# Kernel optimization log

Measured on AMD Instinct MI355X. Metric: run time of the kernel, lower is better.

Reference implementation:

```python
import jax, jax.numpy as jnp
import numpy as np

N = 50000      # total nodes in batched graph
E = 800000     # total edges (avg degree 16)
B = 512        # number of graphs in batch
F_IN = 74      # input node feature size
H = 64         # hidden size per layer
OUT = 64       # output_feats
EPS = 1e-5     # BatchNorm eps


def setup_inputs() -> dict:
    key = jax.random.key(0)
    ks = jax.random.split(key, 32)
    d = {}
    d['feats'] = jax.random.normal(ks[0], (N, F_IN), dtype=jnp.float32)
    d['src'] = jax.random.randint(ks[1], (E,), 0, N)
    d['dst'] = jax.random.randint(ks[2], (E,), 0, N)
    d['graph_ids'] = jnp.sort(jax.random.randint(ks[3], (N,), 0, B))
    dims = [F_IN, H, H, H]
    i = 4
    for l in range(3):
        din, dout = dims[l], dims[l + 1]
        d[f'W{l}'] = jax.random.normal(ks[i], (din, dout), jnp.float32) / np.sqrt(din).astype(np.float32); i += 1
        d[f'b{l}'] = jnp.zeros((dout,), jnp.float32)
        d[f'rW{l}'] = jax.random.normal(ks[i], (din, dout), jnp.float32) / np.sqrt(din).astype(np.float32); i += 1
        d[f'rb{l}'] = jnp.zeros((dout,), jnp.float32)
        d[f'g{l}'] = jnp.ones((dout,), jnp.float32)    # BN gamma
        d[f'be{l}'] = jnp.zeros((dout,), jnp.float32)  # BN beta
    d['aw_W'] = jax.random.normal(ks[i], (H, 1), jnp.float32) / np.sqrt(H).astype(np.float32); i += 1
    d['aw_b'] = jnp.zeros((1,), jnp.float32)
    d['out_W'] = jax.random.normal(ks[i], (2 * H, OUT), jnp.float32) / np.sqrt(2 * H).astype(np.float32); i += 1
    d['out_b'] = jnp.zeros((OUT,), jnp.float32)
    return d


def _gcn_layer(x, src, dst, W, b, rW, rb, g, be):
    # GraphConv, norm='none': out = sum-aggregate(X W) + b, then relu
    xw = x @ W                                                    # [N, dout]
    agg = jax.ops.segment_sum(xw[src], dst, num_segments=N) + b   # gather/scatter over edges
    h = jax.nn.relu(agg)
    # residual: relu(Linear(x))
    h = h + jax.nn.relu(x @ rW + rb)
    # dropout p=0 -> identity
    # BatchNorm1d (training-mode batch statistics, biased variance)
    mean = jnp.mean(h, axis=0)
    var = jnp.var(h, axis=0)
    return (h - mean) * jax.lax.rsqrt(var + EPS) * g + be


def reference(feats, src, dst, graph_ids,
              W0, b0, rW0, rb0, g0, be0,
              W1, b1, rW1, rb1, g1, be1,
              W2, b2, rW2, rb2, g2, be2,
              aw_W, aw_b, out_W, out_b):
    h = feats
    h = _gcn_layer(h, src, dst, W0, b0, rW0, rb0, g0, be0)
    h = _gcn_layer(h, src, dst, W1, b1, rW1, rb1, g1, be1)
    h = _gcn_layer(h, src, dst, W2, b2, rW2, rb2, g2, be2)
    # WeightedSumAndMax readout
    w = jax.nn.sigmoid(h @ aw_W + aw_b)                               # [N, 1]
    h_sum = jax.ops.segment_sum(h * w, graph_ids, num_segments=B)     # [B, H]
    h_max = jax.ops.segment_max(h, graph_ids, num_segments=B)         # [B, H]
    h_max = jnp.where(jnp.isfinite(h_max), h_max, 0.0)                # empty graphs -> 0 (dgl max_nodes)
    h_g = jnp.concatenate([h_sum, h_max], axis=1)                     # [B, 2H]
    return h_g @ out_W + out_b                                        # [B, OUT]
```

## Files before the change

kernel.cpp:

```cpp
#include <hip/hip_runtime.h>
#include <hip/hip_bf16.h>
#include <math.h>

#define NN 50000
#define NE 800000
#define NB 512
#define FIN 74
#define HD 64
#define BN_EPS 1e-5f

#define SCHUNK 512
#define NCHUNK ((NN + SCHUNK - 1) / SCHUNK)

#define CHUNK 32
#define ELLW 32
#define NBLK ((NN + CHUNK - 1) / CHUNK)


__global__ void csr_zero_kernel(int* __restrict__ cnt, int* __restrict__ cnt2,
                                float* __restrict__ stats012,
                                unsigned long long* __restrict__ xw_zrow,
                                const float* __restrict__ W0, const float* __restrict__ rW0,
                                float2* __restrict__ Wpk0) {
    int i = blockIdx.x * 256 + threadIdx.x;
    if (i < NN) { cnt[i] = 0; cnt2[i] = 0; }
    if (i < 384) stats012[i] = 0.f;
    if (i < 16) xw_zrow[i] = 0ull;
    if (i < FIN * HD) Wpk0[i] = make_float2(W0[i], rW0[i]);
}

__global__ void csr_hist_kernel(const int* __restrict__ dst, int* __restrict__ cnt) {
    int e = blockIdx.x * 256 + threadIdx.x;
    if (e < NE) atomicAdd(&cnt[dst[e]], 1);
}

__global__ void scanA_kernel(const int* __restrict__ cnt, int* __restrict__ bsum) {
    __shared__ int l[SCHUNK];
    int i = blockIdx.x * SCHUNK + threadIdx.x;
    int v = (i < NN) ? cnt[i] : 0;
    l[threadIdx.x] = v;
    __syncthreads();
    for (int off = SCHUNK / 2; off; off >>= 1) {
        if (threadIdx.x < off) l[threadIdx.x] += l[threadIdx.x + off];
        __syncthreads();
    }
    if (threadIdx.x == 0) bsum[blockIdx.x] = l[0];
}

__global__ void scanB_kernel(int* __restrict__ bsum) {
    int lane = threadIdx.x;
    int v0 = (lane < NCHUNK) ? bsum[lane] : 0;
    int v1 = (64 + lane < NCHUNK) ? bsum[64 + lane] : 0;
    int s0 = v0, s1 = v1;
    for (int off = 1; off < 64; off <<= 1) {
        int t0 = __shfl_up(s0, off, 64);
        int t1 = __shfl_up(s1, off, 64);
        if (lane >= off) { s0 += t0; s1 += t1; }
    }
    int tot0 = __shfl(s0, 63, 64);
    if (lane < NCHUNK) bsum[lane] = s0 - v0;
    if (64 + lane < NCHUNK) bsum[64 + lane] = s1 - v1 + tot0;
}

__global__ void scanC_kernel(const int* __restrict__ cnt, const int* __restrict__ bsum,
                             int* __restrict__ row_ptr) {
    __shared__ int l[SCHUNK];
    int i = blockIdx.x * SCHUNK + threadIdx.x;
    int v = (i < NN) ? cnt[i] : 0;
    l[threadIdx.x] = v;
    __syncthreads();
    for (int off = 1; off < SCHUNK; off <<= 1) {
        int t = (threadIdx.x >= off) ? l[threadIdx.x - off] : 0;
        __syncthreads();
        l[threadIdx.x] += t;
        __syncthreads();
    }
    int excl = l[threadIdx.x] - v + bsum[blockIdx.x];
    if (i < NN) row_ptr[i] = excl;
    if (i == NN - 1) row_ptr[NN] = excl + v;
}

__global__ void csr_fill_kernel(const int* __restrict__ src, const int* __restrict__ dst,
                                const int* __restrict__ row_ptr, int* __restrict__ cnt2,
                                int* __restrict__ eidx) {
    int i = blockIdx.x * 256 + threadIdx.x;
    if (i < NE) {
        int d = dst[i];
        int p = row_ptr[d] + atomicAdd(&cnt2[d], 1);
        eidx[p] = src[i];
    }
}


template <int K>
__global__ __launch_bounds__(256) void gemm_dual_kernel(
    const float* __restrict__ x, const float2* __restrict__ Wpk,
    const float* __restrict__ rb, __hip_bfloat16* __restrict__ xw,
    __hip_bfloat16* __restrict__ res, int n) {
    __shared__ float2 sW[K * HD];
    __shared__ float srb[64];
    for (int i = threadIdx.x; i < K * HD; i += 256) sW[i] = Wpk[i];
    if (threadIdx.x < 64) srb[threadIdx.x] = rb[threadIdx.x];
    __syncthreads();
    int wl = threadIdx.x >> 6, lane = threadIdx.x & 63;
    for (int r0 = (blockIdx.x * 4 + wl) * 8; r0 < n; r0 += gridDim.x * 32) {
        float a1[8], a2[8];
#pragma unroll
        for (int r = 0; r < 8; ++r) { a1[r] = 0.f; a2[r] = 0.f; }
#pragma unroll
        for (int c0 = 0; c0 < K; c0 += 64) {
            const int cl = (K - c0 < 64) ? (K - c0) : 64;
            float xv[8];
#pragma unroll
            for (int r = 0; r < 8; ++r) {
                int row = r0 + r;
                xv[r] = (lane < cl && row < n) ? x[(size_t)row * K + c0 + lane] : 0.f;
            }
            for (int j = 0; j < cl; ++j) {
                float2 w = sW[(c0 + j) * HD + lane];
#pragma unroll
                for (int r = 0; r < 8; ++r) {
                    float xb = __uint_as_float(
                        __builtin_amdgcn_readlane(__float_as_uint(xv[r]), j));
                    a1[r] = fmaf(xb, w.x, a1[r]);
                    a2[r] = fmaf(xb, w.y, a2[r]);
                }
            }
        }
#pragma unroll
        for (int r = 0; r < 8; ++r) {
            int row = r0 + r;
            if (row < n) {
                xw[(size_t)row * HD + lane] = __float2bfloat16(a1[r]);
                res[(size_t)row * HD + lane] = __float2bfloat16(fmaxf(a2[r] + srb[lane], 0.f));
            }
        }
    }
}

__global__ void fold_kernel(const float* __restrict__ stats, const float* __restrict__ g,
                            const float* __restrict__ be, const float* __restrict__ W,
                            const float* __restrict__ rW, const float* __restrict__ rb,
                            float2* __restrict__ Wpk, float* __restrict__ shiftW,
                            float* __restrict__ rbp) {
    __shared__ float sc[64], sh[64];
    int t = threadIdx.x;
    if (t < 64) {
        float mean = stats[t] / (float)NN;
        float var = stats[64 + t] / (float)NN - mean * mean;
        float scale = g[t] * rsqrtf(var + BN_EPS);
        sc[t] = scale;
        sh[t] = be[t] - mean * scale;
    }
    __syncthreads();
    for (int i = t; i < 64 * 64; i += 256) {
        int k = i >> 6;
        Wpk[i] = make_float2(sc[k] * W[i], sc[k] * rW[i]);
    }
    if (t < 64) {
        float sw = 0.f, srw = 0.f;
        for (int k = 0; k < 64; ++k) {
            sw = fmaf(sh[k], W[k * 64 + t], sw);
            srw = fmaf(sh[k], rW[k * 64 + t], srw);
        }
        shiftW[t] = sw;
        rbp[t] = rb[t] + srw;
    }
}

__device__ __forceinline__ float bf_lo(unsigned int p) { return __uint_as_float(p << 16); }
__device__ __forceinline__ float bf_hi(unsigned int p) { return __uint_as_float(p & 0xffff0000u); }

__global__ __launch_bounds__(256) void fused_agg_kernel(
    const __hip_bfloat16* __restrict__ xw, const __hip_bfloat16* __restrict__ res,
    const float* __restrict__ b, const float* __restrict__ shiftW,
    const int* __restrict__ row_ptr, const int* __restrict__ geidx,
    float* __restrict__ hout, float* __restrict__ stats, int n) {
    __shared__ int sIdx[CHUNK][ELLW];
    __shared__ int sRP[CHUNK + 1];
    __shared__ int sLen[CHUNK];
    __shared__ float sbb[128];
    __shared__ float lsr[256 * 4];

    int tid = threadIdx.x;
    int r0 = blockIdx.x * CHUNK;

    if (tid <= CHUNK) {
        int rp = r0 + tid;
        sRP[tid] = row_ptr[(rp < NN) ? rp : NN];
    }
    if (tid >= 128 && tid < 256) {
        int j = tid - 128;
        sbb[j] = (j < 64) ? b[j] : (shiftW ? shiftW[j - 64] : 0.f);
    }
    __syncthreads();
    for (int i = tid; i < CHUNK * ELLW; i += 256) {
        int r = i >> 5, j = i & 31;
        int beg = sRP[r];
        int plen = sRP[r + 1] - beg;
        sIdx[r][j] = (j < plen) ? geidx[beg + j] : NN;
        if (j == 0) sLen[r] = plen;
    }
    __syncthreads();

    const unsigned* XWdw = (const unsigned*)xw;
    const unsigned* REdw = (const unsigned*)res;
    int wl = tid >> 6, lane = tid & 63;
    int c2 = lane & 31, half = lane >> 5;
    float sb0 = sbb[2 * c2], sb1 = sbb[2 * c2 + 1];
    float sw0 = sbb[64 + 2 * c2], sw1 = sbb[64 + 2 * c2 + 1];
    float s0 = 0.f, s1 = 0.f, q0 = 0.f, q1 = 0.f;

#pragma unroll
    for (int p = 0; p < 4; ++p) {
        int rA = wl * 8 + 2 * p;
        int rloc = rA + half;
        int grow = r0 + rloc;
        int growc = (grow < n) ? grow : (n - 1);
        int lenA = sLen[rA], lenB = sLen[rA + 1];
        int kmax = (lenA > lenB) ? lenA : lenB;
        int mylen = half ? lenB : lenA;
        unsigned rdw = REdw[(size_t)growc * 32 + c2];
        float a0 = 0.f, a1 = 0.f;
        int klim = (kmax < ELLW) ? kmax : ELLW;
        for (int k8 = 0; k8 < klim; k8 += 8) {
#pragma unroll
            for (int j = 0; j < 8; ++j) {
                int idx = sIdx[rloc][k8 + j];
                unsigned dw = XWdw[(size_t)idx * 32 + c2];
                a0 += bf_lo(dw);
                a1 += bf_hi(dw);
            }
        }
        if (kmax > ELLW) {
            int beg = sRP[rloc];
            for (int k = ELLW; k < kmax; ++k) {
                int idx = geidx[beg + k];
                unsigned dw = XWdw[(size_t)((k < mylen) ? idx : NN) * 32 + c2];
                a0 += bf_lo(dw);
                a1 += bf_hi(dw);
            }
        }
        float dg = (float)mylen;
        float hv0 = fmaxf(a0 + fmaf(dg, sw0, sb0), 0.f) + bf_lo(rdw);
        float hv1 = fmaxf(a1 + fmaf(dg, sw1, sb1), 0.f) + bf_hi(rdw);
        if (grow < n) {
            *(float2*)&hout[(size_t)grow * HD + 2 * c2] = make_float2(hv0, hv1);
            s0 += hv0; s1 += hv1;
            q0 += hv0 * hv0; q1 += hv1 * hv1;
        }
    }

    lsr[tid * 4 + 0] = s0;
    lsr[tid * 4 + 1] = s1;
    lsr[tid * 4 + 2] = q0;
    lsr[tid * 4 + 3] = q1;
    __syncthreads();
    if (tid < 64) {
        int comp = tid & 1, c2i = tid >> 1;
        float ss = 0.f, qq = 0.f;
#pragma unroll
        for (int w = 0; w < 4; ++w)
#pragma unroll
            for (int h = 0; h < 2; ++h) {
                int t = w * 64 + h * 32 + c2i;
                ss += lsr[t * 4 + comp];
                qq += lsr[t * 4 + 2 + comp];
            }
        atomicAdd(&stats[tid], ss);
        atomicAdd(&stats[64 + tid], qq);
    }
}


__global__ void readout_init_kernel(float* __restrict__ hsum, unsigned int* __restrict__ hmax,
                                    const float* __restrict__ stats, const float* __restrict__ g,
                                    const float* __restrict__ be, float* __restrict__ ss) {
    int idx = blockIdx.x * 256 + threadIdx.x;
    if (idx < NB * HD) {
        hsum[idx] = 0.f;
        hmax[idx] = 0x007FFFFFu;
    }
    if (blockIdx.x == 0 && threadIdx.x < 64) {
        int c = threadIdx.x;
        float mean = stats[c] / (float)NN;
        float var = stats[64 + c] / (float)NN - mean * mean;
        float scale = g[c] * rsqrtf(var + BN_EPS);
        ss[c] = scale;
        ss[64 + c] = be[c] - mean * scale;
    }
}

#define RNODES 16

__device__ __forceinline__ void ro_flush(float* hsum, unsigned int* hmax, int g, int c,
                                         float accS, float accM) {
    atomicAdd(&hsum[g * HD + c], accS);
    unsigned int bits = __float_as_uint(accM);
    unsigned int enc = (bits & 0x80000000u) ? ~bits : (bits | 0x80000000u);
    atomicMax(&hmax[g * HD + c], enc);
}

__global__ __launch_bounds__(256) void readout_kernel(
    const float* __restrict__ h, const int* __restrict__ gid, const float* __restrict__ ss,
    const float* __restrict__ awW, const float* __restrict__ awb, float* __restrict__ hsum,
    unsigned int* __restrict__ hmax, int n) {
    int wid = blockIdx.x * 4 + (threadIdx.x >> 6);
    int c = threadIdx.x & 63;
    int r0 = wid * RNODES;
    if (r0 >= n) return;
    int r1 = r0 + RNODES;
    if (r1 > n) r1 = n;
    float aw = awW[c], ab = awb[0];
    float sA = ss[c], sB = ss[64 + c];
    int cur = gid[r0];
    float accS = 0.f, accM = -__builtin_inff();
    for (int r = r0; r < r1; ++r) {
        int g = gid[r];
        if (g != cur) {
            ro_flush(hsum, hmax, cur, c, accS, accM);
            accS = 0.f;
            accM = -__builtin_inff();
            cur = g;
        }
        float v = fmaf(h[(size_t)r * HD + c], sA, sB);
        float p = v * aw;
        for (int off = 32; off; off >>= 1) p += __shfl_xor(p, off, 64);
        float w = 1.f / (1.f + expf(-(p + ab)));
        accS = fmaf(v, w, accS);
        accM = fmaxf(accM, v);
    }
    ro_flush(hsum, hmax, cur, c, accS, accM);
}

__global__ void final_kernel(const float* __restrict__ hsum, const unsigned int* __restrict__ hmax,
                             const float* __restrict__ outW, const float* __restrict__ outb,
                             float* __restrict__ out) {
    __shared__ float sW[128 * 64];
    for (int i = threadIdx.x; i < 128 * 64; i += 256) sW[i] = outW[i];
    __syncthreads();
    int idx = blockIdx.x * 256 + threadIdx.x;
    if (idx >= NB * HD) return;
    int bi = idx >> 6, o = idx & 63;
    float acc = outb[o];
#pragma unroll 4
    for (int k = 0; k < 64; ++k) acc = fmaf(hsum[bi * 64 + k], sW[k * 64 + o], acc);
#pragma unroll 4
    for (int k = 0; k < 64; ++k) {
        unsigned int e = hmax[bi * 64 + k];
        float m;
        if (e == 0x007FFFFFu) {
            m = 0.f;
        } else {
            m = (e & 0x80000000u) ? __uint_as_float(e ^ 0x80000000u) : __uint_as_float(~e);
        }
        acc = fmaf(m, sW[(64 + k) * 64 + o], acc);
    }
    out[idx] = acc;
}


extern "C" void kernel_launch(void* const* d_in, const int* in_sizes, int n_in,
                              void* d_out, int out_size, void* d_ws, size_t ws_size,
                              hipStream_t stream) {
    const float* feats = (const float*)d_in[0];
    const int* src = (const int*)d_in[1];
    const int* dst = (const int*)d_in[2];
    const int* gid = (const int*)d_in[3];
    const float* W[3];
    const float* b[3];
    const float* rW[3];
    const float* rb[3];
    const float* g[3];
    const float* be[3];
    for (int l = 0; l < 3; ++l) {
        W[l] = (const float*)d_in[4 + 6 * l + 0];
        b[l] = (const float*)d_in[4 + 6 * l + 1];
        rW[l] = (const float*)d_in[4 + 6 * l + 2];
        rb[l] = (const float*)d_in[4 + 6 * l + 3];
        g[l] = (const float*)d_in[4 + 6 * l + 4];
        be[l] = (const float*)d_in[4 + 6 * l + 5];
    }
    const float* awW = (const float*)d_in[22];
    const float* awb = (const float*)d_in[23];
    const float* outW = (const float*)d_in[24];
    const float* outb = (const float*)d_in[25];
    float* out = (float*)d_out;

    __hip_bfloat16* XW = (__hip_bfloat16*)d_ws;
    __hip_bfloat16* RES = XW + (size_t)(NN + 1) * HD;
    float* P1 = (float*)(RES + (size_t)NN * HD);
    float* stats = P1 + (size_t)NN * HD;
    float* ss2 = stats + 384;
    float2* WPK = (float2*)(ss2 + 128);
    float* shW = (float*)(WPK + FIN * HD);
    float* rbp = shW + 64;
    float* hsum = rbp + 64;
    unsigned int* hmax = (unsigned int*)(hsum + (size_t)NB * HD);
    int* cnt = (int*)(hmax + (size_t)NB * HD);
    int* cnt2 = cnt + NN;
    int* row_ptr = cnt2 + NN;
    int* bsum = row_ptr + NN + 1;
    int* eidx = bsum + NCHUNK;

    float* stats0 = stats;
    float* stats1 = stats + 128;
    float* stats2 = stats + 256;

    const int EBLK = (NE + 255) / 256;
    const int GEMMBLK = 640;
    const int ROBLK = (NN + RNODES * 4 - 1) / (RNODES * 4);

    csr_zero_kernel<<<(NN + 255) / 256, 256, 0, stream>>>(
        cnt, cnt2, stats, (unsigned long long*)(XW + (size_t)NN * HD), W[0], rW[0], WPK);
    csr_hist_kernel<<<EBLK, 256, 0, stream>>>(dst, cnt);
    scanA_kernel<<<NCHUNK, SCHUNK, 0, stream>>>(cnt, bsum);
    scanB_kernel<<<1, 64, 0, stream>>>(bsum);
    scanC_kernel<<<NCHUNK, SCHUNK, 0, stream>>>(cnt, bsum, row_ptr);
    csr_fill_kernel<<<EBLK, 256, 0, stream>>>(src, dst, row_ptr, cnt2, eidx);

    gemm_dual_kernel<FIN><<<GEMMBLK, 256, 0, stream>>>(feats, WPK, rb[0], XW, RES, NN);
    fused_agg_kernel<<<NBLK, 256, 0, stream>>>(XW, RES, b[0], (const float*)nullptr, row_ptr,
                                               eidx, P1, stats0, NN);

    fold_kernel<<<1, 256, 0, stream>>>(stats0, g[0], be[0], W[1], rW[1], rb[1], WPK, shW, rbp);
    gemm_dual_kernel<HD><<<GEMMBLK, 256, 0, stream>>>(P1, WPK, rbp, XW, RES, NN);
    fused_agg_kernel<<<NBLK, 256, 0, stream>>>(XW, RES, b[1], shW, row_ptr, eidx, P1, stats1, NN);

    fold_kernel<<<1, 256, 0, stream>>>(stats1, g[1], be[1], W[2], rW[2], rb[2], WPK, shW, rbp);
    gemm_dual_kernel<HD><<<GEMMBLK, 256, 0, stream>>>(P1, WPK, rbp, XW, RES, NN);
    fused_agg_kernel<<<NBLK, 256, 0, stream>>>(XW, RES, b[2], shW, row_ptr, eidx, P1, stats2, NN);

    readout_init_kernel<<<(NB * HD + 255) / 256, 256, 0, stream>>>(hsum, hmax, stats2, g[2], be[2], ss2);
    readout_kernel<<<ROBLK, 256, 0, stream>>>(P1, gid, ss2, awW, awb, hsum, hmax, NN);
    final_kernel<<<(NB * HD + 255) / 256, 256, 0, stream>>>(hsum, hmax, outW, outb, out);
}
```

Before: 389.2 us.

## Widen aggregation gathers to 8-byte loads and unroll 16-deep with shuffle stats

New measurement: 371.2 us. 1.05x faster.

```diff
diff --git a/kernel.cpp b/kernel.cpp
--- a/kernel.cpp
+++ b/kernel.cpp
@@ -171,16 +171,31 @@
 __device__ __forceinline__ float bf_lo(unsigned int p) { return __uint_as_float(p << 16); }
 __device__ __forceinline__ float bf_hi(unsigned int p) { return __uint_as_float(p & 0xffff0000u); }
 
-__global__ __launch_bounds__(256) void fused_agg_kernel(
+#define GATHER16(BASE)                                             \
+    {                                                              \
+        unsigned long long d[16];                                  \
+        _Pragma("unroll") for (int j = 0; j < 16; ++j) {           \
+            int idx = sIdx[rloc][(BASE) + j];                      \
+            unsigned off = (unsigned)idx * 16u + (unsigned)c8;     \
+            d[j] = XWu[off];                                       \
+        }                                                          \
+        _Pragma("unroll") for (int j = 0; j < 16; ++j) {           \
+            unsigned lo = (unsigned)d[j], hi = (unsigned)(d[j] >> 32); \
+            a0 += bf_lo(lo); a1 += bf_hi(lo);                      \
+            a2 += bf_lo(hi); a3 += bf_hi(hi);                      \
+        }                                                          \
+    }
+
+__global__ __launch_bounds__(256, 4) void fused_agg_kernel(
     const __hip_bfloat16* __restrict__ xw, const __hip_bfloat16* __restrict__ res,
     const float* __restrict__ b, const float* __restrict__ shiftW,
     const int* __restrict__ row_ptr, const int* __restrict__ geidx,
     float* __restrict__ hout, float* __restrict__ stats, int n) {
-    __shared__ int sIdx[CHUNK][ELLW];
+    __shared__ int sIdx[CHUNK][ELLW + 1];
     __shared__ int sRP[CHUNK + 1];
     __shared__ int sLen[CHUNK];
     __shared__ float sbb[128];
-    __shared__ float lsr[256 * 4];
+    __shared__ float lsr[4][16][8];
 
     int tid = threadIdx.x;
     int r0 = blockIdx.x * CHUNK;
@@ -203,72 +218,74 @@
     }
     __syncthreads();
 
-    const unsigned* XWdw = (const unsigned*)xw;
-    const unsigned* REdw = (const unsigned*)res;
+    const unsigned long long* XWu = (const unsigned long long*)xw;
+    const unsigned long long* REu = (const unsigned long long*)res;
     int wl = tid >> 6, lane = tid & 63;
-    int c2 = lane & 31, half = lane >> 5;
-    float sb0 = sbb[2 * c2], sb1 = sbb[2 * c2 + 1];
-    float sw0 = sbb[64 + 2 * c2], sw1 = sbb[64 + 2 * c2 + 1];
-    float s0 = 0.f, s1 = 0.f, q0 = 0.f, q1 = 0.f;
-
-#pragma unroll
-    for (int p = 0; p < 4; ++p) {
-        int rA = wl * 8 + 2 * p;
-        int rloc = rA + half;
+    int q = lane >> 4, c8 = lane & 15;
+    float sb0 = sbb[4 * c8], sb1 = sbb[4 * c8 + 1], sb2 = sbb[4 * c8 + 2], sb3 = sbb[4 * c8 + 3];
+    float sw0 = sbb[64 + 4 * c8], sw1 = sbb[64 + 4 * c8 + 1];
+    float sw2 = sbb[64 + 4 * c8 + 2], sw3 = sbb[64 + 4 * c8 + 3];
+    float s0 = 0.f, s1 = 0.f, s2 = 0.f, s3 = 0.f;
+    float q0 = 0.f, q1 = 0.f, q2 = 0.f, q3 = 0.f;
+
+#pragma unroll
+    for (int p = 0; p < 2; ++p) {
+        int rbase = wl * 8 + p * 4;
+        int rloc = rbase + q;
         int grow = r0 + rloc;
         int growc = (grow < n) ? grow : (n - 1);
-        int lenA = sLen[rA], lenB = sLen[rA + 1];
-        int kmax = (lenA > lenB) ? lenA : lenB;
-        int mylen = half ? lenB : lenA;
-        unsigned rdw = REdw[(size_t)growc * 32 + c2];
-        float a0 = 0.f, a1 = 0.f;
-        int klim = (kmax < ELLW) ? kmax : ELLW;
-        for (int k8 = 0; k8 < klim; k8 += 8) {
-#pragma unroll
-            for (int j = 0; j < 8; ++j) {
-                int idx = sIdx[rloc][k8 + j];
-                unsigned dw = XWdw[(size_t)idx * 32 + c2];
-                a0 += bf_lo(dw);
-                a1 += bf_hi(dw);
-            }
-        }
+        int l0 = sLen[rbase], l1 = sLen[rbase + 1], l2 = sLen[rbase + 2], l3 = sLen[rbase + 3];
+        int m01 = (l0 > l1) ? l0 : l1, m23 = (l2 > l3) ? l2 : l3;
+        int kmax = (m01 > m23) ? m01 : m23;
+        int mylen = sLen[rloc];
+        unsigned long long rqw = REu[(unsigned)growc * 16u + (unsigned)c8];
+        float a0 = 0.f, a1 = 0.f, a2 = 0.f, a3 = 0.f;
+        GATHER16(0)
+        if (kmax > 16) GATHER16(16)
         if (kmax > ELLW) {
             int beg = sRP[rloc];
             for (int k = ELLW; k < kmax; ++k) {
                 int idx = geidx[beg + k];
-                unsigned dw = XWdw[(size_t)((k < mylen) ? idx : NN) * 32 + c2];
-                a0 += bf_lo(dw);
-                a1 += bf_hi(dw);
+                unsigned off = (unsigned)((k < mylen) ? idx : NN) * 16u + (unsigned)c8;
+                unsigned long long u = XWu[off];
+                unsigned lo = (unsigned)u, hi = (unsigned)(u >> 32);
+                a0 += bf_lo(lo); a1 += bf_hi(lo);
+                a2 += bf_lo(hi); a3 += bf_hi(hi);
             }
         }
+        unsigned rlo = (unsigned)rqw, rhi = (unsigned)(rqw >> 32);
         float dg = (float)mylen;
-        float hv0 = fmaxf(a0 + fmaf(dg, sw0, sb0), 0.f) + bf_lo(rdw);
-        float hv1 = fmaxf(a1 + fmaf(dg, sw1, sb1), 0.f) + bf_hi(rdw);
+        float h0 = fmaxf(a0 + fmaf(dg, sw0, sb0), 0.f) + bf_lo(rlo);
+        float h1 = fmaxf(a1 + fmaf(dg, sw1, sb1), 0.f) + bf_hi(rlo);
+        float h2 = fmaxf(a2 + fmaf(dg, sw2, sb2), 0.f) + bf_lo(rhi);
+        float h3 = fmaxf(a3 + fmaf(dg, sw3, sb3), 0.f) + bf_hi(rhi);
         if (grow < n) {
-            *(float2*)&hout[(size_t)grow * HD + 2 * c2] = make_float2(hv0, hv1);
-            s0 += hv0; s1 += hv1;
-            q0 += hv0 * hv0; q1 += hv1 * hv1;
-        }
-    }
-
-    lsr[tid * 4 + 0] = s0;
-    lsr[tid * 4 + 1] = s1;
-    lsr[tid * 4 + 2] = q0;
-    lsr[tid * 4 + 3] = q1;
+            *(float4*)&hout[(unsigned)grow * 64u + 4u * c8] = make_float4(h0, h1, h2, h3);
+            s0 += h0; s1 += h1; s2 += h2; s3 += h3;
+            q0 += h0 * h0; q1 += h1 * h1; q2 += h2 * h2; q3 += h3 * h3;
+        }
+    }
+
+    s0 += __shfl_xor(s0, 16, 64); s0 += __shfl_xor(s0, 32, 64);
+    s1 += __shfl_xor(s1, 16, 64); s1 += __shfl_xor(s1, 32, 64);
+    s2 += __shfl_xor(s2, 16, 64); s2 += __shfl_xor(s2, 32, 64);
+    s3 += __shfl_xor(s3, 16, 64); s3 += __shfl_xor(s3, 32, 64);
+    q0 += __shfl_xor(q0, 16, 64); q0 += __shfl_xor(q0, 32, 64);
+    q1 += __shfl_xor(q1, 16, 64); q1 += __shfl_xor(q1, 32, 64);
+    q2 += __shfl_xor(q2, 16, 64); q2 += __shfl_xor(q2, 32, 64);
+    q3 += __shfl_xor(q3, 16, 64); q3 += __shfl_xor(q3, 32, 64);
+    if (q == 0) {
+        lsr[wl][c8][0] = s0; lsr[wl][c8][1] = s1; lsr[wl][c8][2] = s2; lsr[wl][c8][3] = s3;
+        lsr[wl][c8][4] = q0; lsr[wl][c8][5] = q1; lsr[wl][c8][6] = q2; lsr[wl][c8][7] = q3;
+    }
     __syncthreads();
     if (tid < 64) {
-        int comp = tid & 1, c2i = tid >> 1;
-        float ss = 0.f, qq = 0.f;
-#pragma unroll
-        for (int w = 0; w < 4; ++w)
-#pragma unroll
-            for (int h = 0; h < 2; ++h) {
-                int t = w * 64 + h * 32 + c2i;
-                ss += lsr[t * 4 + comp];
-                qq += lsr[t * 4 + 2 + comp];
-            }
-        atomicAdd(&stats[tid], ss);
-        atomicAdd(&stats[64 + tid], qq);
+        int c8i = tid >> 2, comp = tid & 3;
+        float ssum = lsr[0][c8i][comp] + lsr[1][c8i][comp] + lsr[2][c8i][comp] + lsr[3][c8i][comp];
+        float qsum = lsr[0][c8i][4 + comp] + lsr[1][c8i][4 + comp] + lsr[2][c8i][4 + comp] +
+                     lsr[3][c8i][4 + comp];
+        atomicAdd(&stats[tid], ssum);
+        atomicAdd(&stats[64 + tid], qsum);
     }
 }
 
@@ -408,7 +425,7 @@
     float* stats2 = stats + 256;
 
     const int EBLK = (NE + 255) / 256;
-    const int GEMMBLK = 640;
+    const int GEMMBLK = 1280;
     const int ROBLK = (NN + RNODES * 4 - 1) / (RNODES * 4);
 
     csr_zero_kernel<<<(NN + 255) / 256, 256, 0, stream>>>(
```
